# Kernel tuning notes

Measured on AMD Instinct MI355X. Metric: run time of the kernel, lower is better.

Reference implementation:

```python
import jax, jax.numpy as jnp
import numpy as np

N, E, D, C, M = 50000, 600000, 128, 40, 25000


def setup_inputs() -> dict:
    key = jax.random.key(0)
    ks = jax.random.split(key, 10)
    s = 1.0 / np.sqrt(D)
    return {
        "x": jax.random.normal(ks[0], (N, D), jnp.float32),
        "edge_index": jax.random.randint(ks[1], (2, E), 0, N, jnp.int64),
        "node_label_index": jax.random.randint(ks[2], (M,), 0, N, jnp.int64),
        "W0": jax.random.normal(ks[3], (D, D), jnp.float32) * s,
        "b0": jnp.zeros((D,), jnp.float32),
        "W1": jax.random.normal(ks[4], (D, D), jnp.float32) * s,
        "b1": jnp.zeros((D,), jnp.float32),
        "W2": jax.random.normal(ks[5], (D, D), jnp.float32) * s,
        "b2": jnp.zeros((D,), jnp.float32),
        "W3": jax.random.normal(ks[6], (D, D), jnp.float32) * s,
        "b3": jnp.zeros((D,), jnp.float32),
        "Wh": jax.random.normal(ks[7], (D, C), jnp.float32) * s,
        "bh": jnp.zeros((C,), jnp.float32),
    }


def _gcn(x, W, b, src, dst, dinv):
    h = x @ W                                    # [N, D']
    norm = (dinv[src] * dinv[dst])[:, None]      # [E, 1]
    agg = jax.ops.segment_sum(h[src] * norm, dst, num_segments=x.shape[0])
    return agg + h * (dinv ** 2)[:, None] + b    # self-loop term + bias


def reference(x, edge_index, node_label_index, W0, b0, W1, b1, W2, b2, W3, b3, Wh, bh):
    src, dst = edge_index[0], edge_index[1]
    # degree with self-loops (PyG counts in-degree on dst after add_self_loops)
    deg = 1.0 + jax.ops.segment_sum(jnp.ones((src.shape[0],), x.dtype), dst,
                                    num_segments=x.shape[0])
    dinv = jax.lax.rsqrt(deg)

    cell0 = _gcn(x, W0, b0, src, dst, dinv)
    cell1 = _gcn(jax.nn.relu(cell0), W1, b1, src, dst, dinv)
    cell2 = (_gcn(jax.nn.relu(cell0), W2, b2, src, dst, dinv)
             + _gcn(jax.nn.relu(cell1), W2, b2, src, dst, dinv))
    cell3 = (_gcn(jax.nn.relu(cell0), W3, b3, src, dst, dinv)
             + _gcn(jax.nn.relu(cell1), W3, b3, src, dst, dinv)
             + _gcn(jax.nn.relu(cell2), W3, b3, src, dst, dinv))

    feat = jax.nn.log_softmax(cell3, axis=1)
    pred = (feat @ Wh + bh)[node_label_index]    # [M, C]
    return pred
```

## Files before the change

### kernel.cpp

```cpp
#include <hip/hip_runtime.h>
#include <hip/hip_bf16.h>
#include <cstdint>
#include <cstddef>

#define DIM 128

typedef __attribute__((ext_vector_type(8))) short bf16x8;
typedef __attribute__((ext_vector_type(4))) float f32x4;

__device__ __forceinline__ unsigned short f2bf(float f) {
    __hip_bfloat16 h = __float2bfloat16(f);
    return *(unsigned short*)&h;
}
__device__ __forceinline__ unsigned pack_bf2(float a, float b) {
    return (unsigned)f2bf(a) | ((unsigned)f2bf(b) << 16);
}
__device__ __forceinline__ float bflo(unsigned u) { return __uint_as_float(u << 16); }
__device__ __forceinline__ float bfhi(unsigned u) { return __uint_as_float(u & 0xffff0000u); }

union U4B8 { uint4 q; bf16x8 v; };

__global__ void k_count(const int* __restrict__ dst, int* __restrict__ count, int e) {
    int i = blockIdx.x * 256 + threadIdx.x;
    if (i < e) atomicAdd(&count[dst[i]], 1);
}

__global__ __launch_bounds__(1024)
void k_scanA(const int* __restrict__ count, int* __restrict__ partial,
             int* __restrict__ bsum, float* __restrict__ dinv, int n) {
    __shared__ int wsum[16];
    int tid = threadIdx.x, lane = tid & 63, wid = tid >> 6;
    int i = blockIdx.x * 1024 + tid;
    int v = (i < n) ? count[i] : 0;
    if (i < n) dinv[i] = rsqrtf(1.0f + (float)v);
    int x = v;
    #pragma unroll
    for (int off = 1; off < 64; off <<= 1) {
        int y = __shfl_up(x, off, 64);
        if (lane >= off) x += y;
    }
    if (lane == 63) wsum[wid] = x;
    __syncthreads();
    int waveoff = 0, total = 0;
    #pragma unroll
    for (int w = 0; w < 16; ++w) {
        int s = wsum[w];
        if (w < wid) waveoff += s;
        total += s;
    }
    if (i < n) partial[i] = x + waveoff;
    if (tid == 0) bsum[blockIdx.x] = total;
}

__global__ __launch_bounds__(1024)
void k_scanB(const int* __restrict__ count, const int* __restrict__ partial,
             const int* __restrict__ bsum, int* __restrict__ row_ptr,
             int* __restrict__ cursor, int n, int nb) {
    __shared__ int s_off;
    int tid = threadIdx.x;
    if (tid < 64) {
        int carry = 0;
        for (int base = 0; base < nb; base += 64) {
            int idx = base + tid;
            int v = (idx < nb && idx < blockIdx.x) ? bsum[idx] : 0;
            #pragma unroll
            for (int off = 32; off > 0; off >>= 1) v += __shfl_xor(v, off, 64);
            carry += v;
        }
        if (tid == 0) s_off = carry;
    }
    __syncthreads();
    int off = s_off;
    int i = blockIdx.x * 1024 + tid;
    if (i < n) {
        int inc = partial[i] + off;
        row_ptr[i + 1] = inc;
        cursor[i] = inc - count[i];
    }
    if (blockIdx.x == 0 && tid == 0) row_ptr[0] = 0;
}

__global__ void k_fill(const int* __restrict__ src, const int* __restrict__ dst,
                       int* __restrict__ cursor, int* __restrict__ col, int e) {
    int i = blockIdx.x * 256 + threadIdx.x;
    if (i < e) {
        int d = dst[i];
        int pos = atomicAdd(&cursor[d], 1);
        col[pos] = src[i];
    }
}

__global__ void k_pack(const float* __restrict__ W0, const float* __restrict__ W1,
                       const float* __restrict__ W2, const float* __restrict__ W3,
                       const float* __restrict__ Wh,
                       unsigned short* __restrict__ Wpk,
                       unsigned short* __restrict__ WhP,
                       float* __restrict__ whs, int C) {
    const int NW = 4 * DIM * DIM;
    const int NH = 3 * 4 * 64 * 8;
    int g = blockIdx.x * 256 + threadIdx.x;
    if (g < NW) {
        int j   = g & 7;
        int ln  = (g >> 3) & 63;
        int kc  = (g >> 9) & 3;
        int nt  = (g >> 11) & 7;
        int mat = g >> 14;
        const float* W = (mat == 0) ? W0 : (mat == 1) ? W1 : (mat == 2) ? W2 : W3;
        int k = kc * 32 + (ln >> 4) * 8 + j;
        int nc = nt * 16 + (ln & 15);
        Wpk[g] = f2bf(W[k * DIM + nc]);
    } else if (g < NW + NH) {
        int gg = g - NW;
        int j  = gg & 7;
        int ln = (gg >> 3) & 63;
        int kc = (gg >> 9) & 3;
        int nt = gg >> 11;
        int k  = kc * 32 + (ln >> 4) * 8 + j;
        int nc = nt * 16 + (ln & 15);
        WhP[gg] = (nc < C) ? f2bf(Wh[k * C + nc]) : (unsigned short)0;
    } else if (g < NW + NH + 64) {
        int c = g - NW - NH;
        if (c < C) {
            float s = 0.f;
            for (int d = 0; d < DIM; ++d) s += Wh[d * C + c];
            whs[c] = s;
        }
    }
}

__global__ __launch_bounds__(256)
void k_matmul_f(const float* __restrict__ in, const unsigned short* __restrict__ Wpk,
                const float* __restrict__ dinv, unsigned short* __restrict__ outp, int n) {
    int wv   = threadIdx.x >> 6;
    int lane = threadIdx.x & 63;
    int r0   = blockIdx.x * 64 + wv * 16;
    int m    = lane & 15;
    int quad = lane >> 4;

    bf16x8 afr[4];
    int arow = r0 + m;
    bool rowok = arow < n;
    const float* ap = in + (size_t)arow * DIM + quad * 8;
    #pragma unroll
    for (int kc = 0; kc < 4; ++kc) {
        float4 p0, p1;
        if (rowok) {
            p0 = *(const float4*)(ap + kc * 32);
            p1 = *(const float4*)(ap + kc * 32 + 4);
        } else {
            p0.x = p0.y = p0.z = p0.w = 0.f;
            p1.x = p1.y = p1.z = p1.w = 0.f;
        }
        union { bf16x8 v; unsigned short u[8]; } a;
        a.u[0] = f2bf(p0.x); a.u[1] = f2bf(p0.y);
        a.u[2] = f2bf(p0.z); a.u[3] = f2bf(p0.w);
        a.u[4] = f2bf(p1.x); a.u[5] = f2bf(p1.y);
        a.u[6] = f2bf(p1.z); a.u[7] = f2bf(p1.w);
        afr[kc] = a.v;
    }

    float dsc[4];
    #pragma unroll
    for (int t = 0; t < 4; ++t) {
        int r = r0 + quad * 4 + t;
        dsc[t] = (r < n) ? dinv[r] : 0.f;
    }

    const uint4* wp = (const uint4*)Wpk;
    #pragma unroll
    for (int nt = 0; nt < 8; ++nt) {
        f32x4 acc = {0.f, 0.f, 0.f, 0.f};
        #pragma unroll
        for (int kc = 0; kc < 4; ++kc) {
            U4B8 b; b.q = wp[(nt * 4 + kc) * 64 + lane];
            acc = __builtin_amdgcn_mfma_f32_16x16x32_bf16(afr[kc], b.v, acc, 0, 0, 0);
        }
        int colb = nt * 16 + m;
        #pragma unroll
        for (int t = 0; t < 4; ++t) {
            int r = r0 + quad * 4 + t;
            if (r < n)
                outp[(size_t)r * DIM + colb] = f2bf(dsc[t] * acc[t]);
        }
    }
}

__global__ __launch_bounds__(256)
void k_matmul_b(const unsigned short* __restrict__ in, const unsigned short* __restrict__ Wpk,
                const float* __restrict__ dinv, unsigned short* __restrict__ outp, int n) {
    int wv   = threadIdx.x >> 6;
    int lane = threadIdx.x & 63;
    int r0   = blockIdx.x * 64 + wv * 16;
    int m    = lane & 15;
    int quad = lane >> 4;

    bf16x8 afr[4];
    int arow = r0 + m;
    bool rowok = arow < n;
    const uint4* in16 = (const uint4*)in;
    #pragma unroll
    for (int kc = 0; kc < 4; ++kc) {
        U4B8 a;
        if (rowok) a.q = in16[(size_t)arow * 16 + kc * 4 + quad];
        else { a.q.x = a.q.y = a.q.z = a.q.w = 0u; }
        afr[kc] = a.v;
    }

    float dsc[4];
    #pragma unroll
    for (int t = 0; t < 4; ++t) {
        int r = r0 + quad * 4 + t;
        dsc[t] = (r < n) ? dinv[r] : 0.f;
    }

    const uint4* wp = (const uint4*)Wpk;
    #pragma unroll
    for (int nt = 0; nt < 8; ++nt) {
        f32x4 acc = {0.f, 0.f, 0.f, 0.f};
        #pragma unroll
        for (int kc = 0; kc < 4; ++kc) {
            U4B8 b; b.q = wp[(nt * 4 + kc) * 64 + lane];
            acc = __builtin_amdgcn_mfma_f32_16x16x32_bf16(afr[kc], b.v, acc, 0, 0, 0);
        }
        int colb = nt * 16 + m;
        #pragma unroll
        for (int t = 0; t < 4; ++t) {
            int r = r0 + quad * 4 + t;
            if (r < n)
                outp[(size_t)r * DIM + colb] = f2bf(dsc[t] * acc[t]);
        }
    }
}

__global__ __launch_bounds__(256)
void k_prop(const unsigned short* __restrict__ h, const int* __restrict__ row_ptr,
            const int* __restrict__ col, const float* __restrict__ dinv,
            const float* __restrict__ bias, float bscale,
            const unsigned short* addin, unsigned short* outp, int n) {
    int node = (blockIdx.x * 256 + threadIdx.x) >> 6;
    int lane = threadIdx.x & 63;
    if (node >= n) return;
    int beg = row_ptr[node], end = row_ptr[node + 1];
    float di = dinv[node];
    int qid = lane >> 4;
    int fo  = lane & 15;
    const uint4* h16 = (const uint4*)h;
    float aL0 = 0.f, aH0 = 0.f, aL1 = 0.f, aH1 = 0.f;
    float aL2 = 0.f, aH2 = 0.f, aL3 = 0.f, aH3 = 0.f;
    float bL0 = 0.f, bH0 = 0.f, bL1 = 0.f, bH1 = 0.f;
    float bL2 = 0.f, bH2 = 0.f, bL3 = 0.f, bH3 = 0.f;
    int j = beg + qid;
    int s0 = (j < end) ? col[j] : -1;
    int s1 = (j + 4 < end) ? col[j + 4] : -1;
    while (s0 >= 0) {
        uint4 d0 = h16[((unsigned)s0 << 4) | fo];
        uint4 d1 = {0u, 0u, 0u, 0u};
        if (s1 >= 0) d1 = h16[((unsigned)s1 << 4) | fo];
        int jn = j + 8;
        s0 = (jn < end) ? col[jn] : -1;
        s1 = (jn + 4 < end) ? col[jn + 4] : -1;
        j = jn;
        aL0 += bflo(d0.x); aH0 += bfhi(d0.x);
        aL1 += bflo(d0.y); aH1 += bfhi(d0.y);
        aL2 += bflo(d0.z); aH2 += bfhi(d0.z);
        aL3 += bflo(d0.w); aH3 += bfhi(d0.w);
        bL0 += bflo(d1.x); bH0 += bfhi(d1.x);
        bL1 += bflo(d1.y); bH1 += bfhi(d1.y);
        bL2 += bflo(d1.z); bH2 += bfhi(d1.z);
        bL3 += bflo(d1.w); bH3 += bfhi(d1.w);
    }
    aL0 += bL0; aH0 += bH0; aL1 += bL1; aH1 += bH1;
    aL2 += bL2; aH2 += bH2; aL3 += bL3; aH3 += bH3;
    aL0 += __shfl_xor(aL0, 16, 64); aL0 += __shfl_xor(aL0, 32, 64);
    aH0 += __shfl_xor(aH0, 16, 64); aH0 += __shfl_xor(aH0, 32, 64);
    aL1 += __shfl_xor(aL1, 16, 64); aL1 += __shfl_xor(aL1, 32, 64);
    aH1 += __shfl_xor(aH1, 16, 64); aH1 += __shfl_xor(aH1, 32, 64);
    aL2 += __shfl_xor(aL2, 16, 64); aL2 += __shfl_xor(aL2, 32, 64);
    aH2 += __shfl_xor(aH2, 16, 64); aH2 += __shfl_xor(aH2, 32, 64);
    aL3 += __shfl_xor(aL3, 16, 64); aL3 += __shfl_xor(aL3, 32, 64);
    aH3 += __shfl_xor(aH3, 16, 64); aH3 += __shfl_xor(aH3, 32, 64);
    uint4 sd = h16[((unsigned)node << 4) | fo];
    aL0 += bflo(sd.x); aH0 += bfhi(sd.x);
    aL1 += bflo(sd.y); aH1 += bfhi(sd.y);
    aL2 += bflo(sd.z); aH2 += bfhi(sd.z);
    aL3 += bflo(sd.w); aH3 += bfhi(sd.w);
    if (lane < 16) {
        const float4* b4 = (const float4*)bias;
        float4 bA = b4[2 * fo], bB = b4[2 * fo + 1];
        float r0x = fmaxf(fmaf(bscale, bA.x, di * aL0), 0.f);
        float r0y = fmaxf(fmaf(bscale, bA.y, di * aH0), 0.f);
        float r0z = fmaxf(fmaf(bscale, bA.z, di * aL1), 0.f);
        float r0w = fmaxf(fmaf(bscale, bA.w, di * aH1), 0.f);
        float r1x = fmaxf(fmaf(bscale, bB.x, di * aL2), 0.f);
        float r1y = fmaxf(fmaf(bscale, bB.y, di * aH2), 0.f);
        float r1z = fmaxf(fmaf(bscale, bB.z, di * aL3), 0.f);
        float r1w = fmaxf(fmaf(bscale, bB.w, di * aH3), 0.f);
        size_t base = (size_t)node * 16 + fo;
        if (addin) {
            uint4 av = ((const uint4*)addin)[base];
            r0x += bflo(av.x); r0y += bfhi(av.x);
            r0z += bflo(av.y); r0w += bfhi(av.y);
            r1x += bflo(av.z); r1y += bfhi(av.z);
            r1z += bflo(av.w); r1w += bfhi(av.w);
        }
        uint4 o;
        o.x = pack_bf2(r0x, r0y);
        o.y = pack_bf2(r0z, r0w);
        o.z = pack_bf2(r1x, r1y);
        o.w = pack_bf2(r1z, r1w);
        ((uint4*)outp)[base] = o;
    }
}

__global__ __launch_bounds__(256)
void k_prop_v(const unsigned short* __restrict__ h, const int* __restrict__ row_ptr,
              const int* __restrict__ col, const float* __restrict__ dinv,
              const float* __restrict__ bias, float bscale,
              const int* __restrict__ labels,
              unsigned short* __restrict__ V, float* __restrict__ Lbuf, int m_total) {
    int m = (blockIdx.x * 256 + threadIdx.x) >> 6;
    int lane = threadIdx.x & 63;
    if (m >= m_total) return;
    int node = labels[m];
    int beg = row_ptr[node], end = row_ptr[node + 1];
    float di = dinv[node];
    int qid = lane >> 4, fo = lane & 15;
    const uint4* h16 = (const uint4*)h;
    float aL0 = 0.f, aH0 = 0.f, aL1 = 0.f, aH1 = 0.f;
    float aL2 = 0.f, aH2 = 0.f, aL3 = 0.f, aH3 = 0.f;
    float bL0 = 0.f, bH0 = 0.f, bL1 = 0.f, bH1 = 0.f;
    float bL2 = 0.f, bH2 = 0.f, bL3 = 0.f, bH3 = 0.f;
    int j = beg + qid;
    int s0 = (j < end) ? col[j] : -1;
    int s1 = (j + 4 < end) ? col[j + 4] : -1;
    while (s0 >= 0) {
        uint4 d0 = h16[((unsigned)s0 << 4) | fo];
        uint4 d1 = {0u, 0u, 0u, 0u};
        if (s1 >= 0) d1 = h16[((unsigned)s1 << 4) | fo];
        int jn = j + 8;
        s0 = (jn < end) ? col[jn] : -1;
        s1 = (jn + 4 < end) ? col[jn + 4] : -1;
        j = jn;
        aL0 += bflo(d0.x); aH0 += bfhi(d0.x);
        aL1 += bflo(d0.y); aH1 += bfhi(d0.y);
        aL2 += bflo(d0.z); aH2 += bfhi(d0.z);
        aL3 += bflo(d0.w); aH3 += bfhi(d0.w);
        bL0 += bflo(d1.x); bH0 += bfhi(d1.x);
        bL1 += bflo(d1.y); bH1 += bfhi(d1.y);
        bL2 += bflo(d1.z); bH2 += bfhi(d1.z);
        bL3 += bflo(d1.w); bH3 += bfhi(d1.w);
    }
    aL0 += bL0; aH0 += bH0; aL1 += bL1; aH1 += bH1;
    aL2 += bL2; aH2 += bH2; aL3 += bL3; aH3 += bH3;
    aL0 += __shfl_xor(aL0, 16, 64); aL0 += __shfl_xor(aL0, 32, 64);
    aH0 += __shfl_xor(aH0, 16, 64); aH0 += __shfl_xor(aH0, 32, 64);
    aL1 += __shfl_xor(aL1, 16, 64); aL1 += __shfl_xor(aL1, 32, 64);
    aH1 += __shfl_xor(aH1, 16, 64); aH1 += __shfl_xor(aH1, 32, 64);
    aL2 += __shfl_xor(aL2, 16, 64); aL2 += __shfl_xor(aL2, 32, 64);
    aH2 += __shfl_xor(aH2, 16, 64); aH2 += __shfl_xor(aH2, 32, 64);
    aL3 += __shfl_xor(aL3, 16, 64); aL3 += __shfl_xor(aL3, 32, 64);
    aH3 += __shfl_xor(aH3, 16, 64); aH3 += __shfl_xor(aH3, 32, 64);
    uint4 sd = h16[((unsigned)node << 4) | fo];
    aL0 += bflo(sd.x); aH0 += bfhi(sd.x);
    aL1 += bflo(sd.y); aH1 += bfhi(sd.y);
    aL2 += bflo(sd.z); aH2 += bfhi(sd.z);
    aL3 += bflo(sd.w); aH3 += bfhi(sd.w);
    const float4* b4 = (const float4*)bias;
    float4 bA = b4[2 * fo], bB = b4[2 * fo + 1];
    float v0 = fmaf(bscale, bA.x, di * aL0);
    float v1 = fmaf(bscale, bA.y, di * aH0);
    float v2 = fmaf(bscale, bA.z, di * aL1);
    float v3 = fmaf(bscale, bA.w, di * aH1);
    float v4 = fmaf(bscale, bB.x, di * aL2);
    float v5 = fmaf(bscale, bB.y, di * aH2);
    float v6 = fmaf(bscale, bB.z, di * aL3);
    float v7 = fmaf(bscale, bB.w, di * aH3);
    float mx = fmaxf(fmaxf(fmaxf(v0, v1), fmaxf(v2, v3)),
                     fmaxf(fmaxf(v4, v5), fmaxf(v6, v7)));
    #pragma unroll
    for (int off = 8; off > 0; off >>= 1) mx = fmaxf(mx, __shfl_xor(mx, off, 64));
    float se = expf(v0 - mx) + expf(v1 - mx) + expf(v2 - mx) + expf(v3 - mx)
             + expf(v4 - mx) + expf(v5 - mx) + expf(v6 - mx) + expf(v7 - mx);
    #pragma unroll
    for (int off = 8; off > 0; off >>= 1) se += __shfl_xor(se, off, 64);
    float L = mx + logf(se);
    if (lane < 16) {
        uint4 o;
        o.x = pack_bf2(v0, v1);
        o.y = pack_bf2(v2, v3);
        o.z = pack_bf2(v4, v5);
        o.w = pack_bf2(v6, v7);
        ((uint4*)V)[(size_t)m * 16 + fo] = o;
    }
    if (lane == 0) Lbuf[m] = L;
}

__global__ __launch_bounds__(256)
void k_head(const unsigned short* __restrict__ V, const float* __restrict__ Lbuf,
            const unsigned short* __restrict__ WhP, const float* __restrict__ whs,
            const float* __restrict__ bh, float* __restrict__ outp,
            int m_total, int C) {
    int wv   = threadIdx.x >> 6;
    int lane = threadIdx.x & 63;
    int r0   = blockIdx.x * 64 + wv * 16;
    int m    = lane & 15;
    int quad = lane >> 4;

    bf16x8 afr[4];
    int arow = r0 + m;
    bool rowok = arow < m_total;
    const uint4* v16 = (const uint4*)V;
    #pragma unroll
    for (int kc = 0; kc < 4; ++kc) {
        U4B8 a;
        if (rowok) a.q = v16[(size_t)arow * 16 + kc * 4 + quad];
        else { a.q.x = a.q.y = a.q.z = a.q.w = 0u; }
        afr[kc] = a.v;
    }
    float lv[4];
    #pragma unroll
    for (int t = 0; t < 4; ++t) {
        int r = r0 + quad * 4 + t;
        lv[t] = (r < m_total) ? Lbuf[r] : 0.f;
    }

    const uint4* wp = (const uint4*)WhP;
    #pragma unroll
    for (int nt = 0; nt < 3; ++nt) {
        f32x4 acc = {0.f, 0.f, 0.f, 0.f};
        #pragma unroll
        for (int kc = 0; kc < 4; ++kc) {
            U4B8 b; b.q = wp[(nt * 4 + kc) * 64 + lane];
            acc = __builtin_amdgcn_mfma_f32_16x16x32_bf16(afr[kc], b.v, acc, 0, 0, 0);
        }
        int colc = nt * 16 + m;
        if (colc < C) {
            float wsc = whs[colc], bc = bh[colc];
            #pragma unroll
            for (int t = 0; t < 4; ++t) {
                int r = r0 + quad * 4 + t;
                if (r < m_total)
                    outp[(size_t)r * C + colc] = acc[t] - lv[t] * wsc + bc;
            }
        }
    }
}

extern "C" void kernel_launch(void* const* d_in, const int* in_sizes, int n_in,
                              void* d_out, int out_size, void* d_ws, size_t ws_size,
                              hipStream_t stream) {
    const float* x      = (const float*)d_in[0];
    const int*   edges  = (const int*)d_in[1];
    const int*   labels = (const int*)d_in[2];
    const float* W0 = (const float*)d_in[3];
    const float* b0 = (const float*)d_in[4];
    const float* W1 = (const float*)d_in[5];
    const float* b1 = (const float*)d_in[6];
    const float* W2 = (const float*)d_in[7];
    const float* b2 = (const float*)d_in[8];
    const float* W3 = (const float*)d_in[9];
    const float* b3 = (const float*)d_in[10];
    const float* Wh = (const float*)d_in[11];
    const float* bh = (const float*)d_in[12];
    float* out = (float*)d_out;

    const int N = in_sizes[0] / DIM;
    const int E = in_sizes[1] / 2;
    const int M = in_sizes[2];
    const int C = in_sizes[12];

    char* ws = (char*)d_ws;
    auto alloc = [&](size_t bytes) {
        char* p = ws;
        ws += (bytes + 255) & ~(size_t)255;
        return p;
    };
    float* dinv    = (float*)alloc((size_t)N * 4);
    int*   count   = (int*)  alloc((size_t)N * 4);
    int*   row_ptr = (int*)  alloc((size_t)(N + 1) * 4);
    int*   cursor  = (int*)  alloc((size_t)N * 4);
    int*   partial = (int*)  alloc((size_t)N * 4);
    int*   bsum    = (int*)  alloc(64 * 4);
    int*   col     = (int*)  alloc((size_t)E * 4);
    float* whs     = (float*)alloc(256);
    unsigned short* Wpk = (unsigned short*)alloc((size_t)4 * DIM * DIM * 2);
    unsigned short* WhP = (unsigned short*)alloc((size_t)3 * 4 * 64 * 8 * 2);
    unsigned short* H   = (unsigned short*)alloc((size_t)N * DIM * 2);
    unsigned short* R0  = (unsigned short*)alloc((size_t)N * DIM * 2);
    unsigned short* A   = (unsigned short*)alloc((size_t)N * DIM * 2);
    unsigned short* V   = (unsigned short*)alloc((size_t)M * DIM * 2);
    float* Lbuf         = (float*)alloc((size_t)M * 4);

    const int* src = edges;
    const int* dst = edges + E;

    int egrid  = (E + 255) / 256;
    int sgrid  = (N + 1023) / 1024;
    int mmgrid = (N + 63) / 64;
    int pgrid  = (N + 3) / 4;
    const int FR = DIM * DIM;
    const int NPACK = 4 * FR + 3 * 4 * 64 * 8 + 64;

    hipMemsetAsync(count, 0, (size_t)N * 4, stream);
    k_count<<<egrid, 256, 0, stream>>>(dst, count, E);
    k_scanA<<<sgrid, 1024, 0, stream>>>(count, partial, bsum, dinv, N);
    k_scanB<<<sgrid, 1024, 0, stream>>>(count, partial, bsum, row_ptr, cursor, N, sgrid);
    k_fill <<<egrid, 256, 0, stream>>>(src, dst, cursor, col, E);
    k_pack <<<(NPACK + 255) / 256, 256, 0, stream>>>(W0, W1, W2, W3, Wh, Wpk, WhP, whs, C);

    k_matmul_f<<<mmgrid, 256, 0, stream>>>(x, Wpk + 0 * FR, dinv, H, N);
    k_prop    <<<pgrid, 256, 0, stream>>>(H, row_ptr, col, dinv, b0, 1.f, nullptr, R0, N);
    k_matmul_b<<<mmgrid, 256, 0, stream>>>(R0, Wpk + 1 * FR, dinv, H, N);
    k_prop    <<<pgrid, 256, 0, stream>>>(H, row_ptr, col, dinv, b1, 1.f, R0, A, N);
    k_matmul_b<<<mmgrid, 256, 0, stream>>>(A, Wpk + 2 * FR, dinv, H, N);
    k_prop    <<<pgrid, 256, 0, stream>>>(H, row_ptr, col, dinv, b2, 2.f, A, A, N);
    k_matmul_b<<<mmgrid, 256, 0, stream>>>(A, Wpk + 3 * FR, dinv, H, N);
    k_prop_v  <<<(M + 3) / 4, 256, 0, stream>>>(H, row_ptr, col, dinv, b3, 3.f,
                                                labels, V, Lbuf, M);
    k_head    <<<(M + 63) / 64, 256, 0, stream>>>(V, Lbuf, WhP, whs, bh, out, M, C);
}
```

Measured before the change: 322.0 us.

## Merge setup kernels, fuse CSR fill with first matmul, fuse prop_v with head

Measured after the change: 310.3 us. 1.04x faster.

```diff
diff --git a/kernel.cpp b/kernel.cpp
--- a/kernel.cpp
+++ b/kernel.cpp
@@ -20,85 +20,23 @@
 
 union U4B8 { uint4 q; bf16x8 v; };
 
-__global__ void k_count(const int* __restrict__ dst, int* __restrict__ count, int e) {
-    int i = blockIdx.x * 256 + threadIdx.x;
-    if (i < e) atomicAdd(&count[dst[i]], 1);
-}
-
-__global__ __launch_bounds__(1024)
-void k_scanA(const int* __restrict__ count, int* __restrict__ partial,
-             int* __restrict__ bsum, float* __restrict__ dinv, int n) {
-    __shared__ int wsum[16];
-    int tid = threadIdx.x, lane = tid & 63, wid = tid >> 6;
-    int i = blockIdx.x * 1024 + tid;
-    int v = (i < n) ? count[i] : 0;
-    if (i < n) dinv[i] = rsqrtf(1.0f + (float)v);
-    int x = v;
-    #pragma unroll
-    for (int off = 1; off < 64; off <<= 1) {
-        int y = __shfl_up(x, off, 64);
-        if (lane >= off) x += y;
-    }
-    if (lane == 63) wsum[wid] = x;
-    __syncthreads();
-    int waveoff = 0, total = 0;
-    #pragma unroll
-    for (int w = 0; w < 16; ++w) {
-        int s = wsum[w];
-        if (w < wid) waveoff += s;
-        total += s;
-    }
-    if (i < n) partial[i] = x + waveoff;
-    if (tid == 0) bsum[blockIdx.x] = total;
-}
-
-__global__ __launch_bounds__(1024)
-void k_scanB(const int* __restrict__ count, const int* __restrict__ partial,
-             const int* __restrict__ bsum, int* __restrict__ row_ptr,
-             int* __restrict__ cursor, int n, int nb) {
-    __shared__ int s_off;
-    int tid = threadIdx.x;
-    if (tid < 64) {
-        int carry = 0;
-        for (int base = 0; base < nb; base += 64) {
-            int idx = base + tid;
-            int v = (idx < nb && idx < blockIdx.x) ? bsum[idx] : 0;
-            #pragma unroll
-            for (int off = 32; off > 0; off >>= 1) v += __shfl_xor(v, off, 64);
-            carry += v;
-        }
-        if (tid == 0) s_off = carry;
-    }
-    __syncthreads();
-    int off = s_off;
-    int i = blockIdx.x * 1024 + tid;
-    if (i < n) {
-        int inc = partial[i] + off;
-        row_ptr[i + 1] = inc;
-        cursor[i] = inc - count[i];
-    }
-    if (blockIdx.x == 0 && tid == 0) row_ptr[0] = 0;
-}
-
-__global__ void k_fill(const int* __restrict__ src, const int* __restrict__ dst,
-                       int* __restrict__ cursor, int* __restrict__ col, int e) {
-    int i = blockIdx.x * 256 + threadIdx.x;
-    if (i < e) {
-        int d = dst[i];
-        int pos = atomicAdd(&cursor[d], 1);
-        col[pos] = src[i];
-    }
-}
-
-__global__ void k_pack(const float* __restrict__ W0, const float* __restrict__ W1,
-                       const float* __restrict__ W2, const float* __restrict__ W3,
-                       const float* __restrict__ Wh,
-                       unsigned short* __restrict__ Wpk,
-                       unsigned short* __restrict__ WhP,
-                       float* __restrict__ whs, int C) {
+__global__ __launch_bounds__(256)
+void k_init(const int* __restrict__ dst, int* __restrict__ count, int e, int egrid,
+            const float* __restrict__ W0, const float* __restrict__ W1,
+            const float* __restrict__ W2, const float* __restrict__ W3,
+            const float* __restrict__ Wh,
+            unsigned short* __restrict__ Wpk,
+            unsigned short* __restrict__ WhP,
+            float* __restrict__ whs,
+            unsigned short* __restrict__ H, int n, int C) {
+    if ((int)blockIdx.x < egrid) {
+        int i = blockIdx.x * 256 + threadIdx.x;
+        if (i < e) atomicAdd(&count[dst[i]], 1);
+        return;
+    }
     const int NW = 4 * DIM * DIM;
     const int NH = 3 * 4 * 64 * 8;
-    int g = blockIdx.x * 256 + threadIdx.x;
+    int g = (blockIdx.x - egrid) * 256 + threadIdx.x;
     if (g < NW) {
         int j   = g & 7;
         int ln  = (g >> 3) & 63;
@@ -125,12 +63,82 @@
             for (int d = 0; d < DIM; ++d) s += Wh[d * C + c];
             whs[c] = s;
         }
-    }
+    } else if (g < NW + NH + 64 + 16) {
+        int t = g - (NW + NH + 64);
+        uint4 z; z.x = z.y = z.z = z.w = 0u;
+        ((uint4*)H)[(size_t)n * 16 + t] = z;
+    }
+}
+
+__global__ __launch_bounds__(1024)
+void k_scanA(const int* __restrict__ count, int* __restrict__ partial,
+             int* __restrict__ bsum, float* __restrict__ dinv, int n) {
+    __shared__ int wsum[16];
+    int tid = threadIdx.x, lane = tid & 63, wid = tid >> 6;
+    int i = blockIdx.x * 1024 + tid;
+    int v = (i < n) ? count[i] : 0;
+    if (i < n) dinv[i] = rsqrtf(1.0f + (float)v);
+    int x = v;
+    #pragma unroll
+    for (int off = 1; off < 64; off <<= 1) {
+        int y = __shfl_up(x, off, 64);
+        if (lane >= off) x += y;
+    }
+    if (lane == 63) wsum[wid] = x;
+    __syncthreads();
+    int waveoff = 0, total = 0;
+    #pragma unroll
+    for (int w = 0; w < 16; ++w) {
+        int s = wsum[w];
+        if (w < wid) waveoff += s;
+        total += s;
+    }
+    if (i < n) partial[i] = x + waveoff;
+    if (tid == 0) bsum[blockIdx.x] = total;
+}
+
+__global__ __launch_bounds__(1024)
+void k_scanB(const int* __restrict__ count, const int* __restrict__ partial,
+             const int* __restrict__ bsum, int* __restrict__ row_ptr,
+             int* __restrict__ cursor, int n, int nb) {
+    __shared__ int s_off;
+    int tid = threadIdx.x;
+    if (tid < 64) {
+        int carry = 0;
+        for (int base = 0; base < nb; base += 64) {
+            int idx = base + tid;
+            int v = (idx < nb && idx < blockIdx.x) ? bsum[idx] : 0;
+            #pragma unroll
+            for (int off = 32; off > 0; off >>= 1) v += __shfl_xor(v, off, 64);
+            carry += v;
+        }
+        if (tid == 0) s_off = carry;
+    }
+    __syncthreads();
+    int off = s_off;
+    int i = blockIdx.x * 1024 + tid;
+    if (i < n) {
+        int inc = partial[i] + off;
+        row_ptr[i + 1] = inc;
+        cursor[i] = inc - count[i];
+    }
+    if (blockIdx.x == 0 && tid == 0) row_ptr[0] = 0;
 }
 
 __global__ __launch_bounds__(256)
-void k_matmul_f(const float* __restrict__ in, const unsigned short* __restrict__ Wpk,
-                const float* __restrict__ dinv, unsigned short* __restrict__ outp, int n) {
+void k_fillmm(const float* __restrict__ in, const unsigned short* __restrict__ Wpk,
+              const float* __restrict__ dinv, unsigned short* __restrict__ outp, int n,
+              const int* __restrict__ src, const int* __restrict__ dst,
+              int* __restrict__ cursor, int* __restrict__ colv, int e, int mmg) {
+    if ((int)blockIdx.x >= mmg) {
+        int i = (blockIdx.x - mmg) * 256 + threadIdx.x;
+        if (i < e) {
+            int d = dst[i];
+            int pos = atomicAdd(&cursor[d], 1);
+            colv[pos] = src[i];
+        }
+        return;
+    }
     int wv   = threadIdx.x >> 6;
     int lane = threadIdx.x & 63;
     int r0   = blockIdx.x * 64 + wv * 16;
@@ -236,7 +244,7 @@
 void k_prop(const unsigned short* __restrict__ h, const int* __restrict__ row_ptr,
             const int* __restrict__ col, const float* __restrict__ dinv,
             const float* __restrict__ bias, float bscale,
-            const unsigned short* addin, unsigned short* outp, int n) {
+            const unsigned short* addin, unsigned short* __restrict__ outp, int n) {
     int node = (blockIdx.x * 256 + threadIdx.x) >> 6;
     int lane = threadIdx.x & 63;
     if (node >= n) return;
@@ -245,20 +253,20 @@
     int qid = lane >> 4;
     int fo  = lane & 15;
     const uint4* h16 = (const uint4*)h;
+    uint4 sd = h16[((unsigned)node << 4) | fo];
     float aL0 = 0.f, aH0 = 0.f, aL1 = 0.f, aH1 = 0.f;
     float aL2 = 0.f, aH2 = 0.f, aL3 = 0.f, aH3 = 0.f;
     float bL0 = 0.f, bH0 = 0.f, bL1 = 0.f, bH1 = 0.f;
     float bL2 = 0.f, bH2 = 0.f, bL3 = 0.f, bH3 = 0.f;
     int j = beg + qid;
-    int s0 = (j < end) ? col[j] : -1;
-    int s1 = (j + 4 < end) ? col[j + 4] : -1;
-    while (s0 >= 0) {
+    int s0 = (j < end) ? col[j] : n;
+    int s1 = (j + 4 < end) ? col[j + 4] : n;
+    while (s0 != n) {
         uint4 d0 = h16[((unsigned)s0 << 4) | fo];
-        uint4 d1 = {0u, 0u, 0u, 0u};
-        if (s1 >= 0) d1 = h16[((unsigned)s1 << 4) | fo];
+        uint4 d1 = h16[((unsigned)s1 << 4) | fo];
         int jn = j + 8;
-        s0 = (jn < end) ? col[jn] : -1;
-        s1 = (jn + 4 < end) ? col[jn + 4] : -1;
+        s0 = (jn < end) ? col[jn] : n;
+        s1 = (jn + 4 < end) ? col[jn + 4] : n;
         j = jn;
         aL0 += bflo(d0.x); aH0 += bfhi(d0.x);
         aL1 += bflo(d0.y); aH1 += bfhi(d0.y);
@@ -269,6 +277,8 @@
         bL2 += bflo(d1.z); bH2 += bfhi(d1.z);
         bL3 += bflo(d1.w); bH3 += bfhi(d1.w);
     }
+    uint4 av; av.x = av.y = av.z = av.w = 0u;
+    if (addin) av = ((const uint4*)addin)[(size_t)node * 16 + fo];
     aL0 += bL0; aH0 += bH0; aL1 += bL1; aH1 += bH1;
     aL2 += bL2; aH2 += bH2; aL3 += bL3; aH3 += bH3;
     aL0 += __shfl_xor(aL0, 16, 64); aL0 += __shfl_xor(aL0, 32, 64);
@@ -279,7 +289,6 @@
     aH2 += __shfl_xor(aH2, 16, 64); aH2 += __shfl_xor(aH2, 32, 64);
     aL3 += __shfl_xor(aL3, 16, 64); aL3 += __shfl_xor(aL3, 32, 64);
     aH3 += __shfl_xor(aH3, 16, 64); aH3 += __shfl_xor(aH3, 32, 64);
-    uint4 sd = h16[((unsigned)node << 4) | fo];
     aL0 += bflo(sd.x); aH0 += bfhi(sd.x);
     aL1 += bflo(sd.y); aH1 += bfhi(sd.y);
     aL2 += bflo(sd.z); aH2 += bfhi(sd.z);
@@ -295,14 +304,11 @@
         float r1y = fmaxf(fmaf(bscale, bB.y, di * aH2), 0.f);
         float r1z = fmaxf(fmaf(bscale, bB.z, di * aL3), 0.f);
         float r1w = fmaxf(fmaf(bscale, bB.w, di * aH3), 0.f);
+        r0x += bflo(av.x); r0y += bfhi(av.x);
+        r0z += bflo(av.y); r0w += bfhi(av.y);
+        r1x += bflo(av.z); r1y += bfhi(av.z);
+        r1z += bflo(av.w); r1w += bfhi(av.w);
         size_t base = (size_t)node * 16 + fo;
-        if (addin) {
-            uint4 av = ((const uint4*)addin)[base];
-            r0x += bflo(av.x); r0y += bfhi(av.x);
-            r0z += bflo(av.y); r0w += bfhi(av.y);
-            r1x += bflo(av.z); r1y += bfhi(av.z);
-            r1z += bflo(av.w); r1w += bfhi(av.w);
-        }
         uint4 o;
         o.x = pack_bf2(r0x, r0y);
         o.y = pack_bf2(r0z, r0w);
@@ -312,34 +318,40 @@
     }
 }
 
-__global__ __launch_bounds__(256)
-void k_prop_v(const unsigned short* __restrict__ h, const int* __restrict__ row_ptr,
-              const int* __restrict__ col, const float* __restrict__ dinv,
-              const float* __restrict__ bias, float bscale,
-              const int* __restrict__ labels,
-              unsigned short* __restrict__ V, float* __restrict__ Lbuf, int m_total) {
-    int m = (blockIdx.x * 256 + threadIdx.x) >> 6;
+__global__ __launch_bounds__(1024)
+void k_propv_head(const unsigned short* __restrict__ h, const int* __restrict__ row_ptr,
+                  const int* __restrict__ col, const float* __restrict__ dinv,
+                  const float* __restrict__ bias, float bscale,
+                  const int* __restrict__ labels,
+                  const unsigned short* __restrict__ WhP, const float* __restrict__ whs,
+                  const float* __restrict__ bh, float* __restrict__ outp,
+                  int m_total, int C, int n) {
+    __shared__ uint4 Vs[16 * 17];
+    __shared__ float Ls[16];
+    int wid  = threadIdx.x >> 6;
     int lane = threadIdx.x & 63;
-    if (m >= m_total) return;
-    int node = labels[m];
-    int beg = row_ptr[node], end = row_ptr[node + 1];
+    int m = blockIdx.x * 16 + wid;
+    bool valid = m < m_total;
+    int node = valid ? labels[m] : 0;
+    int beg = 0, end = 0;
+    if (valid) { beg = row_ptr[node]; end = row_ptr[node + 1]; }
     float di = dinv[node];
     int qid = lane >> 4, fo = lane & 15;
     const uint4* h16 = (const uint4*)h;
+    uint4 sd = h16[((unsigned)node << 4) | fo];
     float aL0 = 0.f, aH0 = 0.f, aL1 = 0.f, aH1 = 0.f;
     float aL2 = 0.f, aH2 = 0.f, aL3 = 0.f, aH3 = 0.f;
     float bL0 = 0.f, bH0 = 0.f, bL1 = 0.f, bH1 = 0.f;
     float bL2 = 0.f, bH2 = 0.f, bL3 = 0.f, bH3 = 0.f;
     int j = beg + qid;
-    int s0 = (j < end) ? col[j] : -1;
-    int s1 = (j + 4 < end) ? col[j + 4] : -1;
-    while (s0 >= 0) {
+    int s0 = (j < end) ? col[j] : n;
+    int s1 = (j + 4 < end) ? col[j + 4] : n;
+    while (s0 != n) {
         uint4 d0 = h16[((unsigned)s0 << 4) | fo];
-        uint4 d1 = {0u, 0u, 0u, 0u};
-        if (s1 >= 0) d1 = h16[((unsigned)s1 << 4) | fo];
+        uint4 d1 = h16[((unsigned)s1 << 4) | fo];
         int jn = j + 8;
-        s0 = (jn < end) ? col[jn] : -1;
-        s1 = (jn + 4 < end) ? col[jn + 4] : -1;
+        s0 = (jn < end) ? col[jn] : n;
+        s1 = (jn + 4 < end) ? col[jn + 4] : n;
         j = jn;
         aL0 += bflo(d0.x); aH0 += bfhi(d0.x);
         aL1 += bflo(d0.y); aH1 += bfhi(d0.y);
@@ -360,7 +372,6 @@
     aH2 += __shfl_xor(aH2, 16, 64); aH2 += __shfl_xor(aH2, 32, 64);
     aL3 += __shfl_xor(aL3, 16, 64); aL3 += __shfl_xor(aL3, 32, 64);
     aH3 += __shfl_xor(aH3, 16, 64); aH3 += __shfl_xor(aH3, 32, 64);
-    uint4 sd = h16[((unsigned)node << 4) | fo];
     aL0 += bflo(sd.x); aH0 += bfhi(sd.x);
     aL1 += bflo(sd.y); aH1 += bfhi(sd.y);
     aL2 += bflo(sd.z); aH2 += bfhi(sd.z);
@@ -390,55 +401,34 @@
         o.y = pack_bf2(v2, v3);
         o.z = pack_bf2(v4, v5);
         o.w = pack_bf2(v6, v7);
-        ((uint4*)V)[(size_t)m * 16 + fo] = o;
-    }
-    if (lane == 0) Lbuf[m] = L;
-}
-
-__global__ __launch_bounds__(256)
-void k_head(const unsigned short* __restrict__ V, const float* __restrict__ Lbuf,
-            const unsigned short* __restrict__ WhP, const float* __restrict__ whs,
-            const float* __restrict__ bh, float* __restrict__ outp,
-            int m_total, int C) {
-    int wv   = threadIdx.x >> 6;
-    int lane = threadIdx.x & 63;
-    int r0   = blockIdx.x * 64 + wv * 16;
-    int m    = lane & 15;
-    int quad = lane >> 4;
-
-    bf16x8 afr[4];
-    int arow = r0 + m;
-    bool rowok = arow < m_total;
-    const uint4* v16 = (const uint4*)V;
-    #pragma unroll
-    for (int kc = 0; kc < 4; ++kc) {
-        U4B8 a;
-        if (rowok) a.q = v16[(size_t)arow * 16 + kc * 4 + quad];
-        else { a.q.x = a.q.y = a.q.z = a.q.w = 0u; }
-        afr[kc] = a.v;
-    }
-    float lv[4];
-    #pragma unroll
-    for (int t = 0; t < 4; ++t) {
-        int r = r0 + quad * 4 + t;
-        lv[t] = (r < m_total) ? Lbuf[r] : 0.f;
-    }
-
-    const uint4* wp = (const uint4*)WhP;
-    #pragma unroll
-    for (int nt = 0; nt < 3; ++nt) {
+        Vs[wid * 17 + fo] = o;
+    }
+    if (lane == 0) Ls[wid] = L;
+    __syncthreads();
+    if (wid < 3) {
+        int mm = lane & 15, quad = lane >> 4;
+        bf16x8 afr[4];
+        #pragma unroll
+        for (int kc = 0; kc < 4; ++kc) {
+            U4B8 a; a.q = Vs[mm * 17 + kc * 4 + quad];
+            afr[kc] = a.v;
+        }
+        float lv[4];
+        #pragma unroll
+        for (int t = 0; t < 4; ++t) lv[t] = Ls[quad * 4 + t];
+        const uint4* wp = (const uint4*)WhP;
         f32x4 acc = {0.f, 0.f, 0.f, 0.f};
         #pragma unroll
         for (int kc = 0; kc < 4; ++kc) {
-            U4B8 b; b.q = wp[(nt * 4 + kc) * 64 + lane];
+            U4B8 b; b.q = wp[(wid * 4 + kc) * 64 + lane];
             acc = __builtin_amdgcn_mfma_f32_16x16x32_bf16(afr[kc], b.v, acc, 0, 0, 0);
         }
-        int colc = nt * 16 + m;
+        int colc = wid * 16 + mm;
         if (colc < C) {
             float wsc = whs[colc], bc = bh[colc];
             #pragma unroll
             for (int t = 0; t < 4; ++t) {
-                int r = r0 + quad * 4 + t;
+                int r = blockIdx.x * 16 + quad * 4 + t;
                 if (r < m_total)
                     outp[(size_t)r * C + colc] = acc[t] - lv[t] * wsc + bc;
             }
@@ -485,11 +475,9 @@
     float* whs     = (float*)alloc(256);
     unsigned short* Wpk = (unsigned short*)alloc((size_t)4 * DIM * DIM * 2);
     unsigned short* WhP = (unsigned short*)alloc((size_t)3 * 4 * 64 * 8 * 2);
-    unsigned short* H   = (unsigned short*)alloc((size_t)N * DIM * 2);
+    unsigned short* H   = (unsigned short*)alloc((size_t)(N + 1) * DIM * 2);
     unsigned short* R0  = (unsigned short*)alloc((size_t)N * DIM * 2);
     unsigned short* A   = (unsigned short*)alloc((size_t)N * DIM * 2);
-    unsigned short* V   = (unsigned short*)alloc((size_t)M * DIM * 2);
-    float* Lbuf         = (float*)alloc((size_t)M * 4);
 
     const int* src = edges;
     const int* dst = edges + E;
@@ -499,23 +487,23 @@
     int mmgrid = (N + 63) / 64;
     int pgrid  = (N + 3) / 4;
     const int FR = DIM * DIM;
-    const int NPACK = 4 * FR + 3 * 4 * 64 * 8 + 64;
+    const int NPACK = 4 * FR + 3 * 4 * 64 * 8 + 64 + 16;
+    int packgrid = (NPACK + 255) / 256;
 
     hipMemsetAsync(count, 0, (size_t)N * 4, stream);
-    k_count<<<egrid, 256, 0, stream>>>(dst, count, E);
+    k_init <<<egrid + packgrid, 256, 0, stream>>>(dst, count, E, egrid,
+                                                  W0, W1, W2, W3, Wh,
+                                                  Wpk, WhP, whs, H, N, C);
     k_scanA<<<sgrid, 1024, 0, stream>>>(count, partial, bsum, dinv, N);
     k_scanB<<<sgrid, 1024, 0, stream>>>(count, partial, bsum, row_ptr, cursor, N, sgrid);
-    k_fill <<<egrid, 256, 0, stream>>>(src, dst, cursor, col, E);
-    k_pack <<<(NPACK + 255) / 256, 256, 0, stream>>>(W0, W1, W2, W3, Wh, Wpk, WhP, whs, C);
-
-    k_matmul_f<<<mmgrid, 256, 0, stream>>>(x, Wpk + 0 * FR, dinv, H, N);
+    k_fillmm<<<mmgrid + egrid, 256, 0, stream>>>(x, Wpk, dinv, H, N,
+                                                 src, dst, cursor, col, E, mmgrid);
     k_prop    <<<pgrid, 256, 0, stream>>>(H, row_ptr, col, dinv, b0, 1.f, nullptr, R0, N);
     k_matmul_b<<<mmgrid, 256, 0, stream>>>(R0, Wpk + 1 * FR, dinv, H, N);
     k_prop    <<<pgrid, 256, 0, stream>>>(H, row_ptr, col, dinv, b1, 1.f, R0, A, N);
     k_matmul_b<<<mmgrid, 256, 0, stream>>>(A, Wpk + 2 * FR, dinv, H, N);
     k_prop    <<<pgrid, 256, 0, stream>>>(H, row_ptr, col, dinv, b2, 2.f, A, A, N);
     k_matmul_b<<<mmgrid, 256, 0, stream>>>(A, Wpk + 3 * FR, dinv, H, N);
-    k_prop_v  <<<(M + 3) / 4, 256, 0, stream>>>(H, row_ptr, col, dinv, b3, 3.f,
-                                                labels, V, Lbuf, M);
-    k_head    <<<(M + 63) / 64, 256, 0, stream>>>(V, Lbuf, WhP, whs, bh, out, M, C);
-}
+    k_propv_head<<<(M + 15) / 16, 1024, 0, stream>>>(H, row_ptr, col, dinv, b3, 3.f,
+                                                     labels, WhP, whs, bh, out, M, C, N);
+}
```
